# Optimization experiments

Measured on AMD Instinct MI355X. Metric: run time of the kernel, lower is better.

The kernel has to match this reference:

```python
import jax, jax.numpy as jnp
import numpy as np

B, D, H, DM, O = 8192, 512, 1024, 2048, 256


def setup_inputs() -> dict:
    key = jax.random.key(0)
    ks = jax.random.split(key, 24)
    def rn(k, shape, scale=1.0):
        return jax.random.normal(k, shape, dtype=jnp.float32) * scale
    w = 0.02  # weight init scale
    return {
        "x":  rn(ks[0], (B, D)),
        "h0": rn(ks[1], (B, H), 0.1), "h1": rn(ks[2], (B, H), 0.1),
        "c0": rn(ks[3], (B, H), 0.1), "c1": rn(ks[4], (B, H), 0.1),
        # Bernoulli keep masks with model_prob=1.0 -> all ones
        "m0": jnp.ones((B, H), jnp.float32), "m1": jnp.ones((B, H), jnp.float32),
        # layer 0 gate weights: in = D + H = 1536
        "Wf0": rn(ks[5], (D + H, H), w), "bf0": jnp.full((H,), 0.01, jnp.float32),
        "Wi0": rn(ks[6], (D + H, H), w), "bi0": jnp.full((H,), 0.01, jnp.float32),
        "Wc0": rn(ks[7], (D + H, H), w), "bc0": jnp.full((H,), 0.01, jnp.float32),
        "Wo0": rn(ks[8], (D + H, H), w), "bo0": jnp.full((H,), 0.01, jnp.float32),
        # layer 1 gate weights: in = H + H = 2048
        "Wf1": rn(ks[9],  (2 * H, H), w), "bf1": jnp.full((H,), 0.01, jnp.float32),
        "Wi1": rn(ks[10], (2 * H, H), w), "bi1": jnp.full((H,), 0.01, jnp.float32),
        "Wc1": rn(ks[11], (2 * H, H), w), "bc1": jnp.full((H,), 0.01, jnp.float32),
        "Wo1": rn(ks[12], (2 * H, H), w), "bo1": jnp.full((H,), 0.01, jnp.float32),
        # output MLP: H -> DM -> O (identity activation per default nn.Sequential())
        "Wm1": rn(ks[13], (H, DM), w), "bm1": jnp.full((DM,), 0.01, jnp.float32),
        "Wm2": rn(ks[14], (DM, O), w), "bm2": jnp.full((O,), 0.01, jnp.float32),
    }


def _lstm_cell(comb, c, Wf, bf, Wi, bi, Wc, bc, Wo, bo):
    # fuse the 4 gate GEMMs into one matmul, then split
    W = jnp.concatenate([Wf, Wi, Wc, Wo], axis=1)      # [in, 4H]
    b = jnp.concatenate([bf, bi, bc, bo])               # [4H]
    g = comb @ W + b                                    # [B, 4H]
    f, i, ct, o = jnp.split(g, 4, axis=1)
    c_new = jax.nn.sigmoid(f) * c + jax.nn.sigmoid(i) * jnp.tanh(ct)
    h_new = jax.nn.sigmoid(o) * jnp.tanh(c_new)
    return h_new, c_new


def reference(x, h0, h1, c0, c1, m0, m1,
              Wf0, bf0, Wi0, bi0, Wc0, bc0, Wo0, bo0,
              Wf1, bf1, Wi1, bi1, Wc1, bc1, Wo1, bo1,
              Wm1, bm1, Wm2, bm2):
    # layer 0: combined = cat(input, h0 * mask0)
    comb0 = jnp.concatenate([x, h0 * m0], axis=1)       # [B, D+H]
    h0n, c0n = _lstm_cell(comb0, c0, Wf0, bf0, Wi0, bi0, Wc0, bc0, Wo0, bo0)
    # layer 1: combined = cat(h0_new * mask0, h1 * mask1)
    comb1 = jnp.concatenate([h0n * m0, h1 * m1], axis=1)  # [B, 2H]
    h1n, c1n = _lstm_cell(comb1, c1, Wf1, bf1, Wi1, bi1, Wc1, bc1, Wo1, bo1)
    # output MLP (dropout p=0 is identity; activation is identity Sequential)
    out = (h1n @ Wm1 + bm1) @ Wm2 + bm2                 # [B, O]
    return out, h0n, h1n, c0n, c1n
```

## Files before the change

### kernel.cpp

```cpp
#include <hip/hip_runtime.h>
#include <hip/hip_bf16.h>
#include <cstdint>
#include <cstddef>

#define DI __device__ __forceinline__

typedef __attribute__((ext_vector_type(8))) short short8;
typedef __attribute__((ext_vector_type(4))) float f32x4;

static constexpr int Bb = 8192, Dd = 512, Hh = 1024;

DI short f2b(float f) {
  union { __hip_bfloat16 h; short s; } u;
  u.h = __float2bfloat16(f);
  return u.s;
}

DI float sigm(float x) {
  float e = __builtin_amdgcn_exp2f(-1.4426950408889634f * x);
  return __builtin_amdgcn_rcpf(1.0f + e);
}
DI float tanh_(float x) {
  float xc = fminf(fmaxf(x, -20.0f), 20.0f);
  float e = __builtin_amdgcn_exp2f(-2.8853900817779268f * xc);
  return (1.0f - e) * __builtin_amdgcn_rcpf(1.0f + e);
}

DI void gload16(const void* g, void* l) {
  __builtin_amdgcn_global_load_lds(
      (const __attribute__((address_space(1))) uint32_t*)g,
      (__attribute__((address_space(3))) uint32_t*)l, 16, 0, 0);
}


__global__ void conv_A0(const float* __restrict__ x, const float* __restrict__ h0,
                        const float* __restrict__ m0, short* __restrict__ A0) {
  const int row = blockIdx.x, t = threadIdx.x;
  float v[8];
  if (t < 64) {
    const float4* p = (const float4*)(x + (size_t)row * Dd + t * 8);
    float4 a = p[0], b = p[1];
    v[0] = a.x; v[1] = a.y; v[2] = a.z; v[3] = a.w;
    v[4] = b.x; v[5] = b.y; v[6] = b.z; v[7] = b.w;
  } else {
    const int j = t * 8 - 512;
    const float4* ph = (const float4*)(h0 + (size_t)row * Hh + j);
    const float4* pm = (const float4*)(m0 + (size_t)row * Hh + j);
    float4 a = ph[0], b = ph[1], ma = pm[0], mb = pm[1];
    v[0] = a.x * ma.x; v[1] = a.y * ma.y; v[2] = a.z * ma.z; v[3] = a.w * ma.w;
    v[4] = b.x * mb.x; v[5] = b.y * mb.y; v[6] = b.z * mb.z; v[7] = b.w * mb.w;
  }
  short8 o;
  #pragma unroll
  for (int q = 0; q < 8; q++) o[q] = f2b(v[q]);
  *(short8*)(A0 + (size_t)row * 1536 + t * 8) = o;
}

__global__ void conv_A1hi(const float* __restrict__ h1, const float* __restrict__ m1,
                          short* __restrict__ A1) {
  const int row = blockIdx.x, t = threadIdx.x;
  const int j = t * 8;
  const float4* ph = (const float4*)(h1 + (size_t)row * Hh + j);
  const float4* pm = (const float4*)(m1 + (size_t)row * Hh + j);
  float4 a = ph[0], b = ph[1], ma = pm[0], mb = pm[1];
  float v[8] = {a.x * ma.x, a.y * ma.y, a.z * ma.z, a.w * ma.w,
                b.x * mb.x, b.y * mb.y, b.z * mb.z, b.w * mb.w};
  short8 o;
  #pragma unroll
  for (int q = 0; q < 8; q++) o[q] = f2b(v[q]);
  *(short8*)(A1 + (size_t)row * 2048 + 1024 + j) = o;
}

__global__ void transpose_conv4(const float* __restrict__ s0, const float* __restrict__ s1,
                                const float* __restrict__ s2, const float* __restrict__ s3,
                                short* __restrict__ dst, int N, int K) {
  __shared__ float t[64][65];
  const int g = blockIdx.z;
  const float* src = (g == 0) ? s0 : (g == 1) ? s1 : (g == 2) ? s2 : s3;
  const int k0 = blockIdx.x * 64, n0 = blockIdx.y * 64;
  const int tid = threadIdx.x;
  const int r = tid >> 2, c0 = (tid & 3) * 16;
  const float* s = src + (size_t)(k0 + r) * N + n0 + c0;
  #pragma unroll
  for (int q = 0; q < 16; q += 4) {
    float4 v = *(const float4*)(s + q);
    t[r][c0 + q + 0] = v.x; t[r][c0 + q + 1] = v.y;
    t[r][c0 + q + 2] = v.z; t[r][c0 + q + 3] = v.w;
  }
  __syncthreads();
  const int n = n0 + r;
  const int j = (n >> 4) * 64 + g * 16 + (n & 15);
  short8 o0, o1;
  #pragma unroll
  for (int q = 0; q < 8; q++) o0[q] = f2b(t[c0 + q][r]);
  #pragma unroll
  for (int q = 0; q < 8; q++) o1[q] = f2b(t[c0 + 8 + q][r]);
  short* d = dst + (size_t)j * K + k0 + c0;
  *(short8*)d = o0;
  *((short8*)d + 1) = o1;
}

__global__ void transpose_conv(const float* __restrict__ src, short* __restrict__ dst,
                               int N, int K) {
  __shared__ float t[64][65];
  const int k0 = blockIdx.x * 64, n0 = blockIdx.y * 64;
  const int tid = threadIdx.x;
  const int r = tid >> 2, c0 = (tid & 3) * 16;
  const float* s = src + (size_t)(k0 + r) * N + n0 + c0;
  #pragma unroll
  for (int q = 0; q < 16; q += 4) {
    float4 v = *(const float4*)(s + q);
    t[r][c0 + q + 0] = v.x; t[r][c0 + q + 1] = v.y;
    t[r][c0 + q + 2] = v.z; t[r][c0 + q + 3] = v.w;
  }
  __syncthreads();
  const int n = n0 + r;
  short8 o0, o1;
  #pragma unroll
  for (int q = 0; q < 8; q++) o0[q] = f2b(t[c0 + q][r]);
  #pragma unroll
  for (int q = 0; q < 8; q++) o1[q] = f2b(t[c0 + 8 + q][r]);
  short* d = dst + (size_t)n * K + k0 + c0;
  *(short8*)d = o0;
  *((short8*)d + 1) = o1;
}

__global__ void conv_plain(const float* __restrict__ src, short* __restrict__ dst, int n8) {
  const int id = blockIdx.x * blockDim.x + threadIdx.x;
  if (id >= n8) return;
  const float4* p = (const float4*)(src + (size_t)id * 8);
  float4 a = p[0], b = p[1];
  short8 o;
  o[0] = f2b(a.x); o[1] = f2b(a.y); o[2] = f2b(a.z); o[3] = f2b(a.w);
  o[4] = f2b(b.x); o[5] = f2b(b.y); o[6] = f2b(b.z); o[7] = f2b(b.w);
  *(short8*)(dst + (size_t)id * 8) = o;
}

__global__ void bp_init(const float* __restrict__ bm2, float* __restrict__ bp) {
  bp[threadIdx.x] = bm2[threadIdx.x];
}
__global__ void bp_acc(const float* __restrict__ bm1, const float* __restrict__ Wm2,
                       float* __restrict__ bp) {
  const int o = threadIdx.x;
  const int k0 = blockIdx.x * 64;
  float s = 0.f;
  #pragma unroll 4
  for (int k = 0; k < 64; k++) s += bm1[k0 + k] * Wm2[(size_t)(k0 + k) * 256 + o];
  atomicAdd(&bp[o], s);
}

template <int EPI>
__global__ __launch_bounds__(256) void gemm_bt(
    const short* __restrict__ A, const short* __restrict__ Bt, int K,
    short* __restrict__ Cb, int ldc,
    float* __restrict__ outp, const float* __restrict__ bpv) {
  __shared__ __align__(16) short sA[128 * 32];
  __shared__ __align__(16) short sB[128 * 32];
  const int tid = threadIdx.x;
  const int lane = tid & 63;
  const int wave = tid >> 6;
  const int wm = wave >> 1, wn = wave & 1;
  const int bm = blockIdx.x, bn = blockIdx.y;
  const int lr = lane & 15, lq = lane >> 4;

  f32x4 acc[4][4] = {};

  const short* pA = A + ((size_t)(bm * 128 + (tid >> 2))) * K + (tid & 3) * 8;
  const short* pB = Bt + ((size_t)(bn * 128 + (tid >> 2))) * K + (tid & 3) * 8;
  short* lA = sA + tid * 8;
  short* lB = sB + tid * 8;
  const int aoff = (wm * 64 + lr) * 32 + lq * 8;
  const int boff = (wn * 64 + lr) * 32 + lq * 8;

  for (int k0 = 0; k0 < K; k0 += 32) {
    gload16(pA + k0, lA);
    gload16(pA + (size_t)64 * K + k0, lA + 2048);
    gload16(pB + k0, lB);
    gload16(pB + (size_t)64 * K + k0, lB + 2048);
    __syncthreads();
    short8 af[4], bv[4];
    #pragma unroll
    for (int m = 0; m < 4; m++) af[m] = *(const short8*)&sA[aoff + m * 512];
    #pragma unroll
    for (int n = 0; n < 4; n++) bv[n] = *(const short8*)&sB[boff + n * 512];
    #pragma unroll
    for (int m = 0; m < 4; m++)
      #pragma unroll
      for (int n = 0; n < 4; n++)
        acc[m][n] = __builtin_amdgcn_mfma_f32_16x16x32_bf16(af[m], bv[n], acc[m][n], 0, 0, 0);
    __syncthreads();
  }

  const int crow0 = bm * 128 + wm * 64 + lq * 4;
  const int ccol0 = bn * 128 + wn * 64 + lr;

  if constexpr (EPI == 0) {
    #pragma unroll
    for (int m = 0; m < 4; m++)
      #pragma unroll
      for (int r = 0; r < 4; r++) {
        const int row = crow0 + m * 16 + r;
        #pragma unroll
        for (int n = 0; n < 4; n++)
          Cb[(size_t)row * ldc + ccol0 + n * 16] = f2b(acc[m][n][r]);
      }
  } else {
    float bvv[4];
    #pragma unroll
    for (int n = 0; n < 4; n++) bvv[n] = bpv[ccol0 + n * 16];
    #pragma unroll
    for (int m = 0; m < 4; m++)
      #pragma unroll
      for (int r = 0; r < 4; r++) {
        const int row = crow0 + m * 16 + r;
        #pragma unroll
        for (int n = 0; n < 4; n++)
          outp[(size_t)row * 256 + ccol0 + n * 16] = acc[m][n][r] + bvv[n];
      }
  }
}


#define STA(buf, h, kt) { const short* s_ = gA + (size_t)(h) * 64 * K + (size_t)(kt) * 64; \
    gload16(s_ + aS0, &sA[buf][h][tid * 8]);                                               \
    gload16(s_ + aS1, &sA[buf][h][4096 + tid * 8]); }
#define STB(buf, h, kt) { const short* s_ = gB + (size_t)(h) * 128 * K + (size_t)(kt) * 64; \
    gload16(s_ + bS0, &sB[buf][h][tid * 8]);                                                \
    gload16(s_ + bS1, &sB[buf][h][4096 + tid * 8]); }

#define LDB(buf) {                                                \
    const short* bb = &sB[buf][bh][brb];                          \
    _Pragma("unroll") for (int n = 0; n < 4; n++) {               \
      bv[n][0] = *(const short8*)(bb + n * 1024 + sw0);           \
      bv[n][1] = *(const short8*)(bb + n * 1024 + sw1); } }

#define LDA_(buf, q, av) {                                        \
    const short* ab = &sA[buf][(q) >> 1][arb + ((q) & 1) * 2048]; \
    av[0][0] = *(const short8*)(ab + sw0);                        \
    av[0][1] = *(const short8*)(ab + sw1);                        \
    av[1][0] = *(const short8*)(ab + 1024 + sw0);                 \
    av[1][1] = *(const short8*)(ab + 1024 + sw1); }

#define MM(q, av) {                                               \
    __builtin_amdgcn_s_setprio(1);                                \
    _Pragma("unroll") for (int m = 0; m < 2; m++)                 \
    _Pragma("unroll") for (int n = 0; n < 4; n++) {               \
      acc[2*(q)+m][n] = __builtin_amdgcn_mfma_f32_16x16x32_bf16(av[m][0], bv[n][0], acc[2*(q)+m][n], 0, 0, 0); \
      acc[2*(q)+m][n] = __builtin_amdgcn_mfma_f32_16x16x32_bf16(av[m][1], bv[n][1], acc[2*(q)+m][n], 0, 0, 0); } \
    __builtin_amdgcn_s_setprio(0); }

#define BARR() __builtin_amdgcn_s_barrier()
#define VM6()  asm volatile("s_waitcnt vmcnt(6)")
#define LG8()  asm volatile("s_waitcnt lgkmcnt(8)")
#define LG0()  asm volatile("s_waitcnt lgkmcnt(0)")

#define PH(buf, q, STG, vm) { short8 av[2][2]; LDA_(buf, q, av); STG; \
    if (vm) VM6(); BARR(); LG0(); MM(q, av); BARR(); }

__global__ __launch_bounds__(512, 2) void gemm8_lstm(
    const short* __restrict__ A, const short* __restrict__ Bt, const int K,
    const float* __restrict__ cprev, float* __restrict__ hout,
    float* __restrict__ cout, short* __restrict__ anext, const int ldan,
    const float* __restrict__ mask,
    const float* __restrict__ bF, const float* __restrict__ bI,
    const float* __restrict__ bC, const float* __restrict__ bO) {
  __shared__ __align__(16) short sA[2][2][8192];
  __shared__ __align__(16) short sB[2][2][8192];
  const int tid = threadIdx.x;
  const int lane = tid & 63, wid = tid >> 6;
  const int wr = wid >> 2, wc = wid & 3;
  const int lr = lane & 15, lq = lane >> 4;
  const int bm = blockIdx.x, bn = blockIdx.y;

  const int NT = K >> 6;
  const int NIT = NT >> 1;

  const int r0 = tid >> 3;
  const int csw = (tid & 7) ^ (r0 & 7);
  const int growA0 = ((r0 >> 5) & 1) * 32 + (r0 & 31);
  const int growA1 = 128 + growA0;
  const size_t aS0 = (size_t)growA0 * K + csw * 8;
  const size_t aS1 = (size_t)growA1 * K + csw * 8;
  const size_t bS0 = (size_t)r0 * K + csw * 8;
  const size_t bS1 = (size_t)(r0 + 64) * K + csw * 8;
  const short* gA = A + (size_t)bm * 256 * K;
  const short* gB = Bt + (size_t)bn * 256 * K;

  const int arb = (wr * 64 + lr) * 64;
  const int brb = ((wc & 1) * 64 + lr) * 64;
  const int bh = wc >> 1;
  const int sw0 = ((lq) ^ (lr & 7)) * 8;
  const int sw1 = ((4 + lq) ^ (lr & 7)) * 8;

  f32x4 acc[8][4] = {};
  short8 bv[4][2];

  STB(0, 0, 0); STB(0, 1, 0); STA(0, 0, 0); STA(0, 1, 0);
  STB(1, 0, 1); STB(1, 1, 1); STA(1, 0, 1);
  VM6(); BARR();

  for (int it = 0; it < NIT; ++it) {
    const int k1 = 2 * it + 1;
    int t2 = 2 * it + 2; if (t2 >= NT) t2 = 0;
    int t3 = 2 * it + 3; if (t3 >= NT) t3 = 1;
    { short8 av[2][2]; LDB(0); LDA_(0, 0, av); STA(1, 1, k1);
      LG8(); BARR(); LG0(); MM(0, av); BARR(); }
    PH(0, 1, STB(0, 0, t2), 0);
    PH(0, 2, STB(0, 1, t2), 0);
    PH(0, 3, STA(0, 0, t2), 1);
    { short8 av[2][2]; LDB(1); LDA_(1, 0, av); STA(0, 1, t2);
      LG8(); BARR(); LG0(); MM(0, av); BARR(); }
    PH(1, 1, STB(1, 0, t3), 0);
    PH(1, 2, STB(1, 1, t3), 0);
    PH(1, 3, STA(1, 0, t3), 1);
  }

  const int n = (bn * 4 + wc) * 16 + lr;
  const float bf_ = bF[n], bi_ = bI[n], bc_ = bC[n], bo_ = bO[n];
  const int row0 = bm * 256 + wr * 128 + lq * 4;

  float cp[4], mk[4], cpn[4], mkn[4];
  #pragma unroll
  for (int rr = 0; rr < 4; rr++) {
    const size_t idx = (size_t)(row0 + rr) * 1024 + n;
    cp[rr] = cprev[idx];
    mk[rr] = mask ? mask[idx] : 1.0f;
  }
  #pragma unroll
  for (int mf = 0; mf < 8; mf++) {
    if (mf < 7) {
      #pragma unroll
      for (int rr = 0; rr < 4; rr++) {
        const size_t idx2 = (size_t)(row0 + (mf + 1) * 16 + rr) * 1024 + n;
        cpn[rr] = cprev[idx2];
        mkn[rr] = mask ? mask[idx2] : 1.0f;
      }
    }
    #pragma unroll
    for (int rr = 0; rr < 4; rr++) {
      const int row = row0 + mf * 16 + rr;
      const size_t idx = (size_t)row * 1024 + n;
      const float fg = sigm(acc[mf][0][rr] + bf_);
      const float ig = sigm(acc[mf][1][rr] + bi_);
      const float cg = tanh_(acc[mf][2][rr] + bc_);
      const float og = sigm(acc[mf][3][rr] + bo_);
      const float cn = fg * cp[rr] + ig * cg;
      const float hn = og * tanh_(cn);
      cout[idx] = cn;
      hout[idx] = hn;
      anext[(size_t)row * ldan + n] = f2b(hn * mk[rr]);
    }
    #pragma unroll
    for (int rr = 0; rr < 4; rr++) { cp[rr] = cpn[rr]; mk[rr] = mkn[rr]; }
  }
}


extern "C" void kernel_launch(void* const* d_in, const int* in_sizes, int n_in,
                              void* d_out, int out_size, void* d_ws, size_t ws_size,
                              hipStream_t stream) {
  (void)in_sizes; (void)n_in; (void)out_size; (void)ws_size;
  const float* x   = (const float*)d_in[0];
  const float* h0  = (const float*)d_in[1];
  const float* h1  = (const float*)d_in[2];
  const float* c0  = (const float*)d_in[3];
  const float* c1  = (const float*)d_in[4];
  const float* m0  = (const float*)d_in[5];
  const float* m1  = (const float*)d_in[6];
  const float* Wf0 = (const float*)d_in[7];  const float* bf0 = (const float*)d_in[8];
  const float* Wi0 = (const float*)d_in[9];  const float* bi0 = (const float*)d_in[10];
  const float* Wc0 = (const float*)d_in[11]; const float* bc0 = (const float*)d_in[12];
  const float* Wo0 = (const float*)d_in[13]; const float* bo0 = (const float*)d_in[14];
  const float* Wf1 = (const float*)d_in[15]; const float* bf1 = (const float*)d_in[16];
  const float* Wi1 = (const float*)d_in[17]; const float* bi1 = (const float*)d_in[18];
  const float* Wc1 = (const float*)d_in[19]; const float* bc1 = (const float*)d_in[20];
  const float* Wo1 = (const float*)d_in[21]; const float* bo1 = (const float*)d_in[22];
  const float* Wm1 = (const float*)d_in[23]; const float* bm1 = (const float*)d_in[24];
  const float* Wm2 = (const float*)d_in[25]; const float* bm2 = (const float*)d_in[26];

  float* dout  = (float*)d_out;
  float* out_o = dout;
  float* h0n   = dout + 2097152;
  float* h1n   = h0n + 8388608;
  float* c0n   = h1n + 8388608;
  float* c1n   = c0n + 8388608;

  char* ws = (char*)d_ws;
  short* A0   = (short*)(ws);
  short* A1   = (short*)(ws + 25165824);
  short* A2   = (short*)(ws + 58720256);
  short* WT0  = (short*)(ws + 75497472);
  short* WT1  = (short*)(ws + 88080384);
  short* Wm1b = (short*)(ws + 104857600);
  short* Wm2T = (short*)(ws + 109051904);
  short* WpT  = (short*)(ws + 110100480);
  float* bp   = (float*)(ws + 110624768);

  conv_A0<<<dim3(8192), dim3(192), 0, stream>>>(x, h0, m0, A0);
  conv_A1hi<<<dim3(8192), dim3(128), 0, stream>>>(h1, m1, A1);
  transpose_conv4<<<dim3(24, 16, 4), dim3(256), 0, stream>>>(Wf0, Wi0, Wc0, Wo0, WT0, 1024, 1536);
  transpose_conv4<<<dim3(32, 16, 4), dim3(256), 0, stream>>>(Wf1, Wi1, Wc1, Wo1, WT1, 1024, 2048);
  conv_plain<<<dim3(1024), dim3(256), 0, stream>>>(Wm1, Wm1b, 262144);
  transpose_conv<<<dim3(32, 4), dim3(256), 0, stream>>>(Wm2, Wm2T, 256, 2048);
  bp_init<<<dim3(1), dim3(256), 0, stream>>>(bm2, bp);
  bp_acc<<<dim3(32), dim3(256), 0, stream>>>(bm1, Wm2, bp);

  gemm_bt<0><<<dim3(2, 8), dim3(256), 0, stream>>>(
      Wm2T, Wm1b, 2048, WpT, 1024, nullptr, nullptr);

  gemm8_lstm<<<dim3(32, 16), dim3(512), 0, stream>>>(
      A0, WT0, 1536, c0, h0n, c0n, A1, 2048, m0, bf0, bi0, bc0, bo0);

  gemm8_lstm<<<dim3(32, 16), dim3(512), 0, stream>>>(
      A1, WT1, 2048, c1, h1n, c1n, A2, 1024, nullptr, bf1, bi1, bc1, bo1);

  gemm_bt<1><<<dim3(64, 2), dim3(256), 0, stream>>>(
      A2, WpT, 1024, nullptr, 0, out_o, bp);
}
```

Before: 393.6 us.

## Merge activation conversion kernels, retile output GEMM, halve LSTM GEMM barrier phases

Three unrelated changes. The two activation conversion kernels become one 320-thread launch. The final output GEMM gets its own kernel with a 64-row tile, so 256 blocks launch instead of 128 and fill more CUs. In the main LSTM GEMM loop, two A sub-tiles are loaded and multiplied per barrier phase instead of one, cutting barriers per K step in half. The cost is higher register pressure, fewer overlap points between LDS reads and global staging, and less reuse of B data per block in the output GEMM.

```diff
diff --git a/kernel.cpp b/kernel.cpp
--- a/kernel.cpp
+++ b/kernel.cpp
@@ -33,42 +33,42 @@
 }
 
 
-__global__ void conv_A0(const float* __restrict__ x, const float* __restrict__ h0,
-                        const float* __restrict__ m0, short* __restrict__ A0) {
+__global__ void conv_acts(const float* __restrict__ x, const float* __restrict__ h0,
+                          const float* __restrict__ m0, const float* __restrict__ h1,
+                          const float* __restrict__ m1,
+                          short* __restrict__ A0, short* __restrict__ A1) {
   const int row = blockIdx.x, t = threadIdx.x;
   float v[8];
-  if (t < 64) {
-    const float4* p = (const float4*)(x + (size_t)row * Dd + t * 8);
-    float4 a = p[0], b = p[1];
-    v[0] = a.x; v[1] = a.y; v[2] = a.z; v[3] = a.w;
-    v[4] = b.x; v[5] = b.y; v[6] = b.z; v[7] = b.w;
+  if (t < 192) {
+    if (t < 64) {
+      const float4* p = (const float4*)(x + (size_t)row * Dd + t * 8);
+      float4 a = p[0], b = p[1];
+      v[0] = a.x; v[1] = a.y; v[2] = a.z; v[3] = a.w;
+      v[4] = b.x; v[5] = b.y; v[6] = b.z; v[7] = b.w;
+    } else {
+      const int j = t * 8 - 512;
+      const float4* ph = (const float4*)(h0 + (size_t)row * Hh + j);
+      const float4* pm = (const float4*)(m0 + (size_t)row * Hh + j);
+      float4 a = ph[0], b = ph[1], ma = pm[0], mb = pm[1];
+      v[0] = a.x * ma.x; v[1] = a.y * ma.y; v[2] = a.z * ma.z; v[3] = a.w * ma.w;
+      v[4] = b.x * mb.x; v[5] = b.y * mb.y; v[6] = b.z * mb.z; v[7] = b.w * mb.w;
+    }
+    short8 o;
+    #pragma unroll
+    for (int q = 0; q < 8; q++) o[q] = f2b(v[q]);
+    *(short8*)(A0 + (size_t)row * 1536 + t * 8) = o;
   } else {
-    const int j = t * 8 - 512;
-    const float4* ph = (const float4*)(h0 + (size_t)row * Hh + j);
-    const float4* pm = (const float4*)(m0 + (size_t)row * Hh + j);
+    const int j = (t - 192) * 8;
+    const float4* ph = (const float4*)(h1 + (size_t)row * Hh + j);
+    const float4* pm = (const float4*)(m1 + (size_t)row * Hh + j);
     float4 a = ph[0], b = ph[1], ma = pm[0], mb = pm[1];
     v[0] = a.x * ma.x; v[1] = a.y * ma.y; v[2] = a.z * ma.z; v[3] = a.w * ma.w;
     v[4] = b.x * mb.x; v[5] = b.y * mb.y; v[6] = b.z * mb.z; v[7] = b.w * mb.w;
-  }
-  short8 o;
-  #pragma unroll
-  for (int q = 0; q < 8; q++) o[q] = f2b(v[q]);
-  *(short8*)(A0 + (size_t)row * 1536 + t * 8) = o;
-}
-
-__global__ void conv_A1hi(const float* __restrict__ h1, const float* __restrict__ m1,
-                          short* __restrict__ A1) {
-  const int row = blockIdx.x, t = threadIdx.x;
-  const int j = t * 8;
-  const float4* ph = (const float4*)(h1 + (size_t)row * Hh + j);
-  const float4* pm = (const float4*)(m1 + (size_t)row * Hh + j);
-  float4 a = ph[0], b = ph[1], ma = pm[0], mb = pm[1];
-  float v[8] = {a.x * ma.x, a.y * ma.y, a.z * ma.z, a.w * ma.w,
-                b.x * mb.x, b.y * mb.y, b.z * mb.z, b.w * mb.w};
-  short8 o;
-  #pragma unroll
-  for (int q = 0; q < 8; q++) o[q] = f2b(v[q]);
-  *(short8*)(A1 + (size_t)row * 2048 + 1024 + j) = o;
+    short8 o;
+    #pragma unroll
+    for (int q = 0; q < 8; q++) o[q] = f2b(v[q]);
+    *(short8*)(A1 + (size_t)row * 2048 + 1024 + j) = o;
+  }
 }
 
 __global__ void transpose_conv4(const float* __restrict__ s0, const float* __restrict__ s1,
@@ -149,11 +149,9 @@
   atomicAdd(&bp[o], s);
 }
 
-template <int EPI>
-__global__ __launch_bounds__(256) void gemm_bt(
+__global__ __launch_bounds__(256) void gemm_bt0(
     const short* __restrict__ A, const short* __restrict__ Bt, int K,
-    short* __restrict__ Cb, int ldc,
-    float* __restrict__ outp, const float* __restrict__ bpv) {
+    short* __restrict__ Cb, int ldc) {
   __shared__ __align__(16) short sA[128 * 32];
   __shared__ __align__(16) short sB[128 * 32];
   const int tid = threadIdx.x;
@@ -193,31 +191,68 @@
 
   const int crow0 = bm * 128 + wm * 64 + lq * 4;
   const int ccol0 = bn * 128 + wn * 64 + lr;
-
-  if constexpr (EPI == 0) {
+  #pragma unroll
+  for (int m = 0; m < 4; m++)
+    #pragma unroll
+    for (int r = 0; r < 4; r++) {
+      const int row = crow0 + m * 16 + r;
+      #pragma unroll
+      for (int n = 0; n < 4; n++)
+        Cb[(size_t)row * ldc + ccol0 + n * 16] = f2b(acc[m][n][r]);
+    }
+}
+
+__global__ __launch_bounds__(256) void gemm_out(
+    const short* __restrict__ A, const short* __restrict__ Bt, int K,
+    float* __restrict__ outp, const float* __restrict__ bpv) {
+  __shared__ __align__(16) short sA[64 * 32];
+  __shared__ __align__(16) short sB[128 * 32];
+  const int tid = threadIdx.x;
+  const int lane = tid & 63;
+  const int wn = tid >> 6;
+  const int bm = blockIdx.x, bn = blockIdx.y;
+  const int lr = lane & 15, lq = lane >> 4;
+
+  f32x4 acc[4][2] = {};
+
+  const short* pA = A + ((size_t)(bm * 64 + (tid >> 2))) * K + (tid & 3) * 8;
+  const short* pB = Bt + ((size_t)(bn * 128 + (tid >> 2))) * K + (tid & 3) * 8;
+  short* lA = sA + tid * 8;
+  short* lB = sB + tid * 8;
+  const int boff = (wn * 32 + lr) * 32 + lq * 8;
+
+  for (int k0 = 0; k0 < K; k0 += 32) {
+    gload16(pA + k0, lA);
+    gload16(pB + k0, lB);
+    gload16(pB + (size_t)64 * K + k0, lB + 2048);
+    __syncthreads();
+    short8 af[4], bv[2];
+    #pragma unroll
+    for (int m = 0; m < 4; m++) af[m] = *(const short8*)&sA[(m * 16 + lr) * 32 + lq * 8];
+    #pragma unroll
+    for (int n = 0; n < 2; n++) bv[n] = *(const short8*)&sB[boff + n * 512];
     #pragma unroll
     for (int m = 0; m < 4; m++)
       #pragma unroll
-      for (int r = 0; r < 4; r++) {
-        const int row = crow0 + m * 16 + r;
-        #pragma unroll
-        for (int n = 0; n < 4; n++)
-          Cb[(size_t)row * ldc + ccol0 + n * 16] = f2b(acc[m][n][r]);
-      }
-  } else {
-    float bvv[4];
-    #pragma unroll
-    for (int n = 0; n < 4; n++) bvv[n] = bpv[ccol0 + n * 16];
-    #pragma unroll
-    for (int m = 0; m < 4; m++)
+      for (int n = 0; n < 2; n++)
+        acc[m][n] = __builtin_amdgcn_mfma_f32_16x16x32_bf16(af[m], bv[n], acc[m][n], 0, 0, 0);
+    __syncthreads();
+  }
+
+  const int crow0 = bm * 64 + lq * 4;
+  const int ccol0 = bn * 128 + wn * 32 + lr;
+  float bvv[2];
+  #pragma unroll
+  for (int n = 0; n < 2; n++) bvv[n] = bpv[ccol0 + n * 16];
+  #pragma unroll
+  for (int m = 0; m < 4; m++)
+    #pragma unroll
+    for (int r = 0; r < 4; r++) {
+      const int row = crow0 + m * 16 + r;
       #pragma unroll
-      for (int r = 0; r < 4; r++) {
-        const int row = crow0 + m * 16 + r;
-        #pragma unroll
-        for (int n = 0; n < 4; n++)
-          outp[(size_t)row * 256 + ccol0 + n * 16] = acc[m][n][r] + bvv[n];
-      }
-  }
+      for (int n = 0; n < 2; n++)
+        outp[(size_t)row * 256 + ccol0 + n * 16] = acc[m][n][r] + bvv[n];
+    }
 }
 
 
@@ -251,11 +286,7 @@
 
 #define BARR() __builtin_amdgcn_s_barrier()
 #define VM6()  asm volatile("s_waitcnt vmcnt(6)")
-#define LG8()  asm volatile("s_waitcnt lgkmcnt(8)")
 #define LG0()  asm volatile("s_waitcnt lgkmcnt(0)")
-
-#define PH(buf, q, STG, vm) { short8 av[2][2]; LDA_(buf, q, av); STG; \
-    if (vm) VM6(); BARR(); LG0(); MM(q, av); BARR(); }
 
 __global__ __launch_bounds__(512, 2) void gemm8_lstm(
     const short* __restrict__ A, const short* __restrict__ Bt, const int K,
@@ -303,16 +334,20 @@
     const int k1 = 2 * it + 1;
     int t2 = 2 * it + 2; if (t2 >= NT) t2 = 0;
     int t3 = 2 * it + 3; if (t3 >= NT) t3 = 1;
-    { short8 av[2][2]; LDB(0); LDA_(0, 0, av); STA(1, 1, k1);
-      LG8(); BARR(); LG0(); MM(0, av); BARR(); }
-    PH(0, 1, STB(0, 0, t2), 0);
-    PH(0, 2, STB(0, 1, t2), 0);
-    PH(0, 3, STA(0, 0, t2), 1);
-    { short8 av[2][2]; LDB(1); LDA_(1, 0, av); STA(0, 1, t2);
-      LG8(); BARR(); LG0(); MM(0, av); BARR(); }
-    PH(1, 1, STB(1, 0, t3), 0);
-    PH(1, 2, STB(1, 1, t3), 0);
-    PH(1, 3, STA(1, 0, t3), 1);
+    { short8 av0[2][2], av1[2][2];
+      LDB(0); LDA_(0, 0, av0); LDA_(0, 1, av1); STA(1, 1, k1);
+      BARR(); LG0(); MM(0, av0); MM(1, av1); BARR(); }
+    { short8 av0[2][2], av1[2][2];
+      LDA_(0, 2, av0); LDA_(0, 3, av1);
+      STB(0, 0, t2); STB(0, 1, t2); STA(0, 0, t2);
+      VM6(); BARR(); LG0(); MM(2, av0); MM(3, av1); BARR(); }
+    { short8 av0[2][2], av1[2][2];
+      LDB(1); LDA_(1, 0, av0); LDA_(1, 1, av1); STA(0, 1, t2);
+      BARR(); LG0(); MM(0, av0); MM(1, av1); BARR(); }
+    { short8 av0[2][2], av1[2][2];
+      LDA_(1, 2, av0); LDA_(1, 3, av1);
+      STB(1, 0, t3); STB(1, 1, t3); STA(1, 0, t3);
+      VM6(); BARR(); LG0(); MM(2, av0); MM(3, av1); BARR(); }
   }
 
   const int n = (bn * 4 + wc) * 16 + lr;
@@ -396,8 +431,7 @@
   short* WpT  = (short*)(ws + 110100480);
   float* bp   = (float*)(ws + 110624768);
 
-  conv_A0<<<dim3(8192), dim3(192), 0, stream>>>(x, h0, m0, A0);
-  conv_A1hi<<<dim3(8192), dim3(128), 0, stream>>>(h1, m1, A1);
+  conv_acts<<<dim3(8192), dim3(320), 0, stream>>>(x, h0, m0, h1, m1, A0, A1);
   transpose_conv4<<<dim3(24, 16, 4), dim3(256), 0, stream>>>(Wf0, Wi0, Wc0, Wo0, WT0, 1024, 1536);
   transpose_conv4<<<dim3(32, 16, 4), dim3(256), 0, stream>>>(Wf1, Wi1, Wc1, Wo1, WT1, 1024, 2048);
   conv_plain<<<dim3(1024), dim3(256), 0, stream>>>(Wm1, Wm1b, 262144);
@@ -405,8 +439,7 @@
   bp_init<<<dim3(1), dim3(256), 0, stream>>>(bm2, bp);
   bp_acc<<<dim3(32), dim3(256), 0, stream>>>(bm1, Wm2, bp);
 
-  gemm_bt<0><<<dim3(2, 8), dim3(256), 0, stream>>>(
-      Wm2T, Wm1b, 2048, WpT, 1024, nullptr, nullptr);
+  gemm_bt0<<<dim3(2, 8), dim3(256), 0, stream>>>(Wm2T, Wm1b, 2048, WpT, 1024);
 
   gemm8_lstm<<<dim3(32, 16), dim3(512), 0, stream>>>(
       A0, WT0, 1536, c0, h0n, c0n, A1, 2048, m0, bf0, bi0, bc0, bo0);
@@ -414,6 +447,5 @@
   gemm8_lstm<<<dim3(32, 16), dim3(512), 0, stream>>>(
       A1, WT1, 2048, c1, h1n, c1n, A2, 1024, nullptr, bf1, bi1, bc1, bo1);
 
-  gemm_bt<1><<<dim3(64, 2), dim3(256), 0, stream>>>(
-      A2, WpT, 1024, nullptr, 0, out_o, bp);
-}
+  gemm_out<<<dim3(128, 2), dim3(256), 0, stream>>>(A2, WpT, 1024, out_o, bp);
+}
```

Measured after the change: 406.6 us. 3.3% more time.
